# Performance work log

Measured on AMD Instinct MI355X. Metric: run time of the kernel, lower is better.

The kernel has to match this reference:

```python
import jax, jax.numpy as jnp
import numpy as np

VOCAB, EDIM, WFEAT, LABELS, SLOPE = 50000, 128, 128, 2, 0.01
N = 8192

def setup_inputs() -> dict:
    key = jax.random.key(0)
    ks = jax.random.split(key, 8)
    inSen = jax.random.randint(ks[0], (N,), 0, VOCAB, dtype=jnp.int64) if jax.config.read('jax_enable_x64') else jax.random.randint(ks[0], (N,), 0, VOCAB, dtype=jnp.int32)
    adj = jax.random.randint(ks[1], (N, N), 0, 2, dtype=jnp.int32)
    emb = jax.random.normal(ks[2], (VOCAB, EDIM), dtype=jnp.float32)
    W = jax.random.normal(ks[3], (EDIM, WFEAT), dtype=jnp.float32) * (1.0 / np.sqrt(EDIM))
    a_src = jax.random.normal(ks[4], (WFEAT,), dtype=jnp.float32) * (1.0 / np.sqrt(WFEAT))
    a_dst = jax.random.normal(ks[5], (WFEAT,), dtype=jnp.float32) * (1.0 / np.sqrt(WFEAT))
    cls_W = jax.random.normal(ks[6], (WFEAT, LABELS), dtype=jnp.float32) * (1.0 / np.sqrt(WFEAT))
    cls_b = jax.random.normal(ks[7], (LABELS,), dtype=jnp.float32) * 0.01
    return {"inSen": inSen, "adj": adj, "selfLink": 1, "emb": emb, "W": W,
            "a_src": a_src, "a_dst": a_dst, "cls_W": cls_W, "cls_b": cls_b}

def reference(inSen, adj, selfLink, emb, W, a_src, a_dst, cls_W, cls_b):
    # Embedding lookup: (N, edim)
    words = emb[inSen]
    # GAT layer: linear projection then adjacency-masked additive attention
    h = words @ W                              # (N, wFeat)
    f_src = h @ a_src                          # (N,)
    f_dst = h @ a_dst                          # (N,)
    e = jax.nn.leaky_relu(f_src[:, None] + f_dst[None, :], negative_slope=SLOPE)  # (N, N)
    mask = (adj + selfLink * jnp.eye(adj.shape[0], dtype=adj.dtype)) > 0
    e = jnp.where(mask, e, jnp.float32(-1e9))
    attention = jax.nn.softmax(e, axis=1)      # (N, N)
    sentence = attention @ h                   # (N, wFeat)
    # Max pool over words, classify
    poolSentence = jnp.max(sentence, axis=0)   # (wFeat,)
    label = jax.nn.softmax(poolSentence @ cls_W + cls_b, axis=0)  # (labels,)
    return (poolSentence, attention, sentence, label)
```

## Files before the change

kernel.cpp:

```cpp
#include <hip/hip_runtime.h>
#include <hip/hip_bf16.h>

#define NR 8192
#define WF 128
#define MSTRIDE 260

typedef short bf16x8 __attribute__((ext_vector_type(8)));
typedef float f32x4 __attribute__((ext_vector_type(4)));

static __device__ __forceinline__ unsigned int f2bf(float f) {
    unsigned int u = __float_as_uint(f);
    return (u + 0x7fffu + ((u >> 16) & 1u)) >> 16;
}
static __device__ __forceinline__ void atomicMaxF(float* addr, float v) {
    if (v >= 0.f) atomicMax((int*)addr, __float_as_int(v));
    else          atomicMin((unsigned int*)addr, __float_as_uint(v));
}
static __device__ __forceinline__ float lrelu(float x) { return x > 0.f ? x : 0.01f * x; }

__global__ __launch_bounds__(256) void k_proj(
    const int* __restrict__ inSen, const float* __restrict__ emb,
    const float* __restrict__ W, const float* __restrict__ a_src,
    const float* __restrict__ a_dst, float* __restrict__ f_src,
    float* __restrict__ f_dst, float* __restrict__ maxfd,
    unsigned short* __restrict__ hB)
{
    __shared__ float ht[16 * 132];
    const int t = threadIdx.x;
    const int f = t & 127, rh = t >> 7;
    const int i0 = blockIdx.x * 16;

    int wd[8];
    #pragma unroll
    for (int r = 0; r < 8; ++r) wd[r] = inSen[i0 + rh * 8 + r];
    float h[8];
    #pragma unroll
    for (int r = 0; r < 8; ++r) h[r] = 0.f;

    for (int k4 = 0; k4 < 32; ++k4) {
        const float w0 = W[(k4 * 4 + 0) * WF + f];
        const float w1 = W[(k4 * 4 + 1) * WF + f];
        const float w2 = W[(k4 * 4 + 2) * WF + f];
        const float w3 = W[(k4 * 4 + 3) * WF + f];
        #pragma unroll
        for (int r = 0; r < 8; ++r) {
            float4 ev = ((const float4*)(emb + (size_t)wd[r] * 128))[k4];
            h[r] += ev.x * w0 + ev.y * w1 + ev.z * w2 + ev.w * w3;
        }
    }
    #pragma unroll
    for (int r = 0; r < 8; ++r) ht[(rh * 8 + r) * 132 + f] = h[r];
    __syncthreads();

    if (t < 16) {
        float s = 0.f, d = 0.f;
        for (int k4 = 0; k4 < 32; ++k4) {
            float4 hv = *(const float4*)(ht + t * 132 + k4 * 4);
            float4 as = ((const float4*)a_src)[k4];
            float4 ad = ((const float4*)a_dst)[k4];
            s += hv.x * as.x + hv.y * as.y + hv.z * as.z + hv.w * as.w;
            d += hv.x * ad.x + hv.y * ad.y + hv.z * ad.z + hv.w * ad.w;
        }
        f_src[i0 + t] = s;
        f_dst[i0 + t] = d;
        float dm = d;
        #pragma unroll
        for (int o = 1; o < 16; o <<= 1) dm = fmaxf(dm, __shfl_xor(dm, o));
        if (t == 0) atomicMaxF(maxfd, dm);
    }
    {
        const int kb = blockIdx.x >> 1, half = blockIdx.x & 1;
        const int nf = t >> 5, l32 = t & 31;
        const int qloc = l32 >> 4, fx = l32 & 15;
        const int lane = (half * 2 + qloc) * 16 + fx;
        const float* hp = ht + (qloc * 8) * 132 + nf * 16 + fx;
        uint4 v;
        v.x = f2bf(hp[0 * 132]) | (f2bf(hp[1 * 132]) << 16);
        v.y = f2bf(hp[2 * 132]) | (f2bf(hp[3 * 132]) << 16);
        v.z = f2bf(hp[4 * 132]) | (f2bf(hp[5 * 132]) << 16);
        v.w = f2bf(hp[6 * 132]) | (f2bf(hp[7 * 132]) << 16);
        *(uint4*)(hB + ((size_t)kb * 8 + nf) * 512 + lane * 8) = v;
    }
}

static __device__ __forceinline__ void adj_chunk(
    int c, int4 a, const float* __restrict__ fdl, int lane, int row, int sl,
    float fs, float C, int shl,
    unsigned int* __restrict__ mrow, float& sum)
{
    const float4 f = *(const float4*)(fdl + c * 256 + 4 * lane);
    const bool m0 = a.x > 0, m1 = a.y > 0, m2 = a.z > 0, m3 = a.w > 0;
    float p0 = m0 ? __expf(lrelu(fs + f.x) - C) : 0.f;
    float p1 = m1 ? __expf(lrelu(fs + f.y) - C) : 0.f;
    float p2 = m2 ? __expf(lrelu(fs + f.z) - C) : 0.f;
    float p3 = m3 ? __expf(lrelu(fs + f.w) - C) : 0.f;
    unsigned int nib = (m0 ? 1u : 0u) | (m1 ? 2u : 0u) | (m2 ? 4u : 0u) | (m3 ? 8u : 0u);
    float ssum = p0 + p1 + p2 + p3;
    if (c == (row >> 8)) {
        if (lane == ((row & 255) >> 2)) {
            const int jd = row & 3;
            const int aj = jd == 0 ? a.x : jd == 1 ? a.y : jd == 2 ? a.z : a.w;
            const float fj = jd == 0 ? f.x : jd == 1 ? f.y : jd == 2 ? f.z : f.w;
            const bool mo = aj > 0, mn = (aj + sl) > 0;
            if (mn != mo) {
                const float pd = __expf(lrelu(fs + fj) - C);
                if (mn) { nib |= 1u << jd; ssum += pd; }
                else    { nib &= ~(1u << jd); ssum -= pd; }
            }
        }
    }
    sum += ssum;
    unsigned int v = nib << shl;
    v |= __shfl_xor(v, 1);
    v |= __shfl_xor(v, 2);
    v |= __shfl_xor(v, 4);
    if ((lane & 7) == 0) mrow[c * 8 + (lane >> 3)] = v;
}

static __device__ __forceinline__ float adj_row(
    const int* __restrict__ ap, const float* __restrict__ fdl,
    int lane, int row, int sl, float fs, float C, int shl,
    unsigned int* __restrict__ mrow,
    int4 a0, int4 a1, int4 a2, int4 a3, int4 a4, int4 a5, int4 a6, int4 a7)
{
    float sum = 0.f;
    #define ADJC(c, reg) adj_chunk((c), (reg), fdl, lane, row, sl, fs, C, shl, mrow, sum)
    #pragma unroll 1
    for (int g = 0; g < 24; g += 8) {
        ADJC(g + 0, a0); a0 = *(const int4*)(ap + (g +  8) * 256);
        ADJC(g + 1, a1); a1 = *(const int4*)(ap + (g +  9) * 256);
        ADJC(g + 2, a2); a2 = *(const int4*)(ap + (g + 10) * 256);
        ADJC(g + 3, a3); a3 = *(const int4*)(ap + (g + 11) * 256);
        ADJC(g + 4, a4); a4 = *(const int4*)(ap + (g + 12) * 256);
        ADJC(g + 5, a5); a5 = *(const int4*)(ap + (g + 13) * 256);
        ADJC(g + 6, a6); a6 = *(const int4*)(ap + (g + 14) * 256);
        ADJC(g + 7, a7); a7 = *(const int4*)(ap + (g + 15) * 256);
    }
    ADJC(24, a0); ADJC(25, a1); ADJC(26, a2); ADJC(27, a3);
    ADJC(28, a4); ADJC(29, a5); ADJC(30, a6); ADJC(31, a7);
    #undef ADJC
    return sum;
}

__global__ __launch_bounds__(512, 4) void k_fused(
    const int* __restrict__ adj, const int* __restrict__ slP,
    const float* __restrict__ f_src, const float* __restrict__ f_dst,
    const float* __restrict__ maxfd, const unsigned short* __restrict__ hB,
    float* __restrict__ att, float* __restrict__ sent, float* __restrict__ partial)
{
    __shared__ float red[8][2048];
    __shared__ float sums[16];
    float* fdl = &red[0][0];
    unsigned int* mask = (unsigned int*)&red[4][0];
    const int t = threadIdx.x, lane = t & 63, w = t >> 6;
    const int strip = blockIdx.x;
    const int i0 = strip * 16;

    const int rowA = i0 + 2 * w;
    const int* __restrict__ apA = adj + (size_t)rowA * NR + 4 * lane;
    int4 a0 = *(const int4*)(apA + 0 * 256);
    int4 a1 = *(const int4*)(apA + 1 * 256);
    int4 a2 = *(const int4*)(apA + 2 * 256);
    int4 a3 = *(const int4*)(apA + 3 * 256);
    int4 a4 = *(const int4*)(apA + 4 * 256);
    int4 a5 = *(const int4*)(apA + 5 * 256);
    int4 a6 = *(const int4*)(apA + 6 * 256);
    int4 a7 = *(const int4*)(apA + 7 * 256);

    #pragma unroll
    for (int i = 0; i < 4; ++i)
        *(float4*)(fdl + (i * 512 + t) * 4) = *(const float4*)(f_dst + (i * 512 + t) * 4);

    const int sl = slP[0];
    const float mfd = maxfd[0];
    const int shl = 4 * (lane & 7);
    __syncthreads();

    {
        const float fsA = f_src[rowA];
        const float CA = lrelu(fsA + mfd);
        float s = adj_row(apA, fdl, lane, rowA, sl, fsA, CA, shl,
                          mask + (2 * w) * MSTRIDE, a0, a1, a2, a3, a4, a5, a6, a7);
        #pragma unroll
        for (int o = 1; o < 64; o <<= 1) s += __shfl_xor(s, o);
        if (lane == 0) sums[2 * w] = 1.0f / s;
    }
    {
        const int rowB = i0 + 2 * w + 1;
        const int* __restrict__ apB = adj + (size_t)rowB * NR + 4 * lane;
        int4 b0 = *(const int4*)(apB + 0 * 256);
        int4 b1 = *(const int4*)(apB + 1 * 256);
        int4 b2 = *(const int4*)(apB + 2 * 256);
        int4 b3 = *(const int4*)(apB + 3 * 256);
        int4 b4 = *(const int4*)(apB + 4 * 256);
        int4 b5 = *(const int4*)(apB + 5 * 256);
        int4 b6 = *(const int4*)(apB + 6 * 256);
        int4 b7 = *(const int4*)(apB + 7 * 256);
        const float fsB = f_src[rowB];
        const float CB = lrelu(fsB + mfd);
        float s = adj_row(apB, fdl, lane, rowB, sl, fsB, CB, shl,
                          mask + (2 * w + 1) * MSTRIDE, b0, b1, b2, b3, b4, b5, b6, b7);
        #pragma unroll
        for (int o = 1; o < 64; o <<= 1) s += __shfl_xor(s, o);
        if (lane == 0) sums[2 * w + 1] = 1.0f / s;
    }
    __syncthreads();

    const int fx = lane & 15, quad = lane >> 4;
    const int row = i0 + fx;
    const float fs = f_src[row];
    const float C = lrelu(fs + mfd);
    const float il = sums[fx];
    float* __restrict__ ar = att + (size_t)row * NR;
    const unsigned int* __restrict__ mrow = mask + fx * MSTRIDE;
    f32x4 acc[8] = {};
    const int k0 = w * 1024;

    for (int kk4 = k0; kk4 < k0 + 1024; kk4 += 128) {
        const uint4 mw = *(const uint4*)(mrow + (kk4 >> 5));
        const unsigned int mwa[4] = {mw.x, mw.y, mw.z, mw.w};
        #pragma unroll
        for (int j4 = 0; j4 < 4; ++j4) {
            const int kk = kk4 + j4 * 32;
            const int kb = kk >> 5;
            const unsigned short* hp = hB + (size_t)kb * 4096 + lane * 8;
            bf16x8 bfr[8];
            #pragma unroll
            for (int nf = 0; nf < 8; ++nf) bfr[nf] = *(const bf16x8*)(hp + nf * 512);

            const unsigned int mbyte = (mwa[j4] >> (quad * 8)) & 0xffu;
            const float4 fd0 = *(const float4*)(fdl + kk + quad * 8);
            const float4 fd1 = *(const float4*)(fdl + kk + quad * 8 + 4);
            const float fv[8] = {fd0.x, fd0.y, fd0.z, fd0.w, fd1.x, fd1.y, fd1.z, fd1.w};
            float p[8];
            #pragma unroll
            for (int j = 0; j < 8; ++j)
                p[j] = ((mbyte >> j) & 1u) ? __expf(lrelu(fs + fv[j]) - C) : 0.f;

            const float4 w0 = make_float4(p[0] * il, p[1] * il, p[2] * il, p[3] * il);
            const float4 w1 = make_float4(p[4] * il, p[5] * il, p[6] * il, p[7] * il);
            *(float4*)(ar + kk + quad * 8) = w0;
            *(float4*)(ar + kk + quad * 8 + 4) = w1;

            union { uint4 u; bf16x8 v; } cv;
            cv.u.x = f2bf(p[0]) | (f2bf(p[1]) << 16);
            cv.u.y = f2bf(p[2]) | (f2bf(p[3]) << 16);
            cv.u.z = f2bf(p[4]) | (f2bf(p[5]) << 16);
            cv.u.w = f2bf(p[6]) | (f2bf(p[7]) << 16);
            #pragma unroll
            for (int nf = 0; nf < 8; ++nf)
                acc[nf] = __builtin_amdgcn_mfma_f32_16x16x32_bf16(cv.v, bfr[nf], acc[nf], 0, 0, 0);
        }
    }
    __syncthreads();
    #pragma unroll
    for (int reg = 0; reg < 4; ++reg) {
        #pragma unroll
        for (int nf = 0; nf < 8; ++nf)
            red[w][(quad * 4 + reg) * 128 + nf * 16 + fx] = acc[nf][reg];
    }
    __syncthreads();
    const int e0 = t * 4;
    const int m = e0 >> 7, f0 = e0 & 127;
    {
        const float vin = sums[m];
        float vv[4];
        #pragma unroll
        for (int j = 0; j < 4; ++j) {
            float s = 0.f;
            #pragma unroll
            for (int sx = 0; sx < 8; ++sx) s += red[sx][e0 + j];
            vv[j] = s * vin;
        }
        *(float4*)(sent + (size_t)(i0 + m) * WF + f0) = make_float4(vv[0], vv[1], vv[2], vv[3]);
        red[0][e0 + 0] = vv[0]; red[0][e0 + 1] = vv[1];
        red[0][e0 + 2] = vv[2]; red[0][e0 + 3] = vv[3];
    }
    __syncthreads();
    if (t < 128) {
        float mx = red[0][t];
        #pragma unroll
        for (int mm = 1; mm < 16; ++mm) mx = fmaxf(mx, red[0][mm * 128 + t]);
        partial[strip * 128 + t] = mx;
    }
}

__global__ __launch_bounds__(128) void k_label(
    const float* __restrict__ partial, const float* __restrict__ cls_W,
    const float* __restrict__ cls_b, float* __restrict__ pool,
    float* __restrict__ label)
{
    __shared__ float s0[128], s1[128];
    const int t = threadIdx.x;
    float m0 = -1e30f, m1 = -1e30f, m2 = -1e30f, m3 = -1e30f;
    for (int b = 0; b < 512; b += 4) {
        m0 = fmaxf(m0, partial[(b + 0) * 128 + t]);
        m1 = fmaxf(m1, partial[(b + 1) * 128 + t]);
        m2 = fmaxf(m2, partial[(b + 2) * 128 + t]);
        m3 = fmaxf(m3, partial[(b + 3) * 128 + t]);
    }
    const float m = fmaxf(fmaxf(m0, m1), fmaxf(m2, m3));
    pool[t] = m;
    s0[t] = m * cls_W[t * 2 + 0];
    s1[t] = m * cls_W[t * 2 + 1];
    __syncthreads();
    if (t == 0) {
        float z0 = cls_b[0], z1 = cls_b[1];
        for (int f = 0; f < 128; ++f) { z0 += s0[f]; z1 += s1[f]; }
        float mm = fmaxf(z0, z1);
        float e0 = __expf(z0 - mm), e1 = __expf(z1 - mm);
        float inv = 1.0f / (e0 + e1);
        label[0] = e0 * inv;
        label[1] = e1 * inv;
    }
}

extern "C" void kernel_launch(void* const* d_in, const int* in_sizes, int n_in,
                              void* d_out, int out_size, void* d_ws, size_t ws_size,
                              hipStream_t stream)
{
    const int*   inSen    = (const int*)d_in[0];
    const int*   adj      = (const int*)d_in[1];
    const int*   selfLink = (const int*)d_in[2];
    const float* emb      = (const float*)d_in[3];
    const float* W        = (const float*)d_in[4];
    const float* a_src    = (const float*)d_in[5];
    const float* a_dst    = (const float*)d_in[6];
    const float* cls_W    = (const float*)d_in[7];
    const float* cls_b    = (const float*)d_in[8];

    float* out   = (float*)d_out;
    float* pool  = out;
    float* att   = out + 128;
    float* sent  = att + (size_t)NR * NR;
    float* label = sent + (size_t)NR * WF;

    char* ws = (char*)d_ws;
    unsigned short* hB    = (unsigned short*)ws;
    float* f_src   = (float*)(ws + (2u << 20));
    float* f_dst   = f_src + NR;
    float* maxfd   = f_dst + NR;
    float* partial = maxfd + 64;

    hipMemsetAsync(maxfd, 0xFF, 4, stream);
    k_proj<<<NR / 16, 256, 0, stream>>>(inSen, emb, W, a_src, a_dst, f_src, f_dst, maxfd, hB);
    k_fused<<<NR / 16, 512, 0, stream>>>(adj, selfLink, f_src, f_dst, maxfd, hB, att, sent, partial);
    k_label<<<1, 128, 0, stream>>>(partial, cls_W, cls_b, pool, label);
}
```

Baseline: 585.8 us.

## Double block size to 32 rows, use nontemporal adj loads and atomic LDS reduction

The fused kernel now runs 1024 threads per block covering 32 rows, so each f_dst staging into LDS is shared by twice as many rows and the grid is halved. The adjacency loads use nontemporal builtins to avoid polluting cache with the streamed 256MB matrix. The cross-wave reduction of MFMA accumulators now uses LDS atomicAdd into two 16-row tiles instead of a staged buffer plus explicit sum. The trade-offs are LDS atomic contention, larger LDS use (about 74KB) that may limit residency, and launch_bounds(1024,4) that may be unachievable.

```diff
diff --git a/kernel.cpp b/kernel.cpp
--- a/kernel.cpp
+++ b/kernel.cpp
@@ -7,6 +7,7 @@
 
 typedef short bf16x8 __attribute__((ext_vector_type(8)));
 typedef float f32x4 __attribute__((ext_vector_type(4)));
+typedef int   i32x4 __attribute__((ext_vector_type(4)));
 
 static __device__ __forceinline__ unsigned int f2bf(float f) {
     unsigned int u = __float_as_uint(f);
@@ -84,12 +85,12 @@
 }
 
 static __device__ __forceinline__ void adj_chunk(
-    int c, int4 a, const float* __restrict__ fdl, int lane, int row, int sl,
+    int c, i32x4 a, const float* __restrict__ fdl, int lane, int row, int sl,
     float fs, float C, int shl,
     unsigned int* __restrict__ mrow, float& sum)
 {
     const float4 f = *(const float4*)(fdl + c * 256 + 4 * lane);
-    const bool m0 = a.x > 0, m1 = a.y > 0, m2 = a.z > 0, m3 = a.w > 0;
+    const bool m0 = a[0] > 0, m1 = a[1] > 0, m2 = a[2] > 0, m3 = a[3] > 0;
     float p0 = m0 ? __expf(lrelu(fs + f.x) - C) : 0.f;
     float p1 = m1 ? __expf(lrelu(fs + f.y) - C) : 0.f;
     float p2 = m2 ? __expf(lrelu(fs + f.z) - C) : 0.f;
@@ -99,7 +100,7 @@
     if (c == (row >> 8)) {
         if (lane == ((row & 255) >> 2)) {
             const int jd = row & 3;
-            const int aj = jd == 0 ? a.x : jd == 1 ? a.y : jd == 2 ? a.z : a.w;
+            const int aj = jd == 0 ? a[0] : jd == 1 ? a[1] : jd == 2 ? a[2] : a[3];
             const float fj = jd == 0 ? f.x : jd == 1 ? f.y : jd == 2 ? f.z : f.w;
             const bool mo = aj > 0, mn = (aj + sl) > 0;
             if (mn != mo) {
@@ -117,24 +118,26 @@
     if ((lane & 7) == 0) mrow[c * 8 + (lane >> 3)] = v;
 }
 
+#define NTL(p) __builtin_nontemporal_load((const i32x4*)(p))
+
 static __device__ __forceinline__ float adj_row(
     const int* __restrict__ ap, const float* __restrict__ fdl,
     int lane, int row, int sl, float fs, float C, int shl,
     unsigned int* __restrict__ mrow,
-    int4 a0, int4 a1, int4 a2, int4 a3, int4 a4, int4 a5, int4 a6, int4 a7)
+    i32x4 a0, i32x4 a1, i32x4 a2, i32x4 a3, i32x4 a4, i32x4 a5, i32x4 a6, i32x4 a7)
 {
     float sum = 0.f;
     #define ADJC(c, reg) adj_chunk((c), (reg), fdl, lane, row, sl, fs, C, shl, mrow, sum)
     #pragma unroll 1
     for (int g = 0; g < 24; g += 8) {
-        ADJC(g + 0, a0); a0 = *(const int4*)(ap + (g +  8) * 256);
-        ADJC(g + 1, a1); a1 = *(const int4*)(ap + (g +  9) * 256);
-        ADJC(g + 2, a2); a2 = *(const int4*)(ap + (g + 10) * 256);
-        ADJC(g + 3, a3); a3 = *(const int4*)(ap + (g + 11) * 256);
-        ADJC(g + 4, a4); a4 = *(const int4*)(ap + (g + 12) * 256);
-        ADJC(g + 5, a5); a5 = *(const int4*)(ap + (g + 13) * 256);
-        ADJC(g + 6, a6); a6 = *(const int4*)(ap + (g + 14) * 256);
-        ADJC(g + 7, a7); a7 = *(const int4*)(ap + (g + 15) * 256);
+        ADJC(g + 0, a0); a0 = NTL(ap + (g +  8) * 256);
+        ADJC(g + 1, a1); a1 = NTL(ap + (g +  9) * 256);
+        ADJC(g + 2, a2); a2 = NTL(ap + (g + 10) * 256);
+        ADJC(g + 3, a3); a3 = NTL(ap + (g + 11) * 256);
+        ADJC(g + 4, a4); a4 = NTL(ap + (g + 12) * 256);
+        ADJC(g + 5, a5); a5 = NTL(ap + (g + 13) * 256);
+        ADJC(g + 6, a6); a6 = NTL(ap + (g + 14) * 256);
+        ADJC(g + 7, a7); a7 = NTL(ap + (g + 15) * 256);
     }
     ADJC(24, a0); ADJC(25, a1); ADJC(26, a2); ADJC(27, a3);
     ADJC(28, a4); ADJC(29, a5); ADJC(30, a6); ADJC(31, a7);
@@ -142,34 +145,37 @@
     return sum;
 }
 
-__global__ __launch_bounds__(512, 4) void k_fused(
+__global__ __launch_bounds__(1024, 4) void k_fused(
     const int* __restrict__ adj, const int* __restrict__ slP,
     const float* __restrict__ f_src, const float* __restrict__ f_dst,
     const float* __restrict__ maxfd, const unsigned short* __restrict__ hB,
     float* __restrict__ att, float* __restrict__ sent, float* __restrict__ partial)
 {
-    __shared__ float red[8][2048];
-    __shared__ float sums[16];
-    float* fdl = &red[0][0];
-    unsigned int* mask = (unsigned int*)&red[4][0];
+    __shared__ float fdl[NR];
+    __shared__ unsigned int mask[32 * MSTRIDE];
+    __shared__ float tile[2][2048];
+    __shared__ float sums[32];
     const int t = threadIdx.x, lane = t & 63, w = t >> 6;
-    const int strip = blockIdx.x;
-    const int i0 = strip * 16;
+    const int i0 = blockIdx.x * 32;
 
     const int rowA = i0 + 2 * w;
     const int* __restrict__ apA = adj + (size_t)rowA * NR + 4 * lane;
-    int4 a0 = *(const int4*)(apA + 0 * 256);
-    int4 a1 = *(const int4*)(apA + 1 * 256);
-    int4 a2 = *(const int4*)(apA + 2 * 256);
-    int4 a3 = *(const int4*)(apA + 3 * 256);
-    int4 a4 = *(const int4*)(apA + 4 * 256);
-    int4 a5 = *(const int4*)(apA + 5 * 256);
-    int4 a6 = *(const int4*)(apA + 6 * 256);
-    int4 a7 = *(const int4*)(apA + 7 * 256);
-
-    #pragma unroll
-    for (int i = 0; i < 4; ++i)
-        *(float4*)(fdl + (i * 512 + t) * 4) = *(const float4*)(f_dst + (i * 512 + t) * 4);
+    i32x4 a0 = NTL(apA + 0 * 256);
+    i32x4 a1 = NTL(apA + 1 * 256);
+    i32x4 a2 = NTL(apA + 2 * 256);
+    i32x4 a3 = NTL(apA + 3 * 256);
+    i32x4 a4 = NTL(apA + 4 * 256);
+    i32x4 a5 = NTL(apA + 5 * 256);
+    i32x4 a6 = NTL(apA + 6 * 256);
+    i32x4 a7 = NTL(apA + 7 * 256);
+
+    #pragma unroll
+    for (int i = 0; i < 2; ++i)
+        *(float4*)(fdl + (i * 1024 + t) * 4) = *(const float4*)(f_dst + (i * 1024 + t) * 4);
+    {
+        float4 z = make_float4(0.f, 0.f, 0.f, 0.f);
+        *(float4*)(&tile[0][0] + t * 4) = z;
+    }
 
     const int sl = slP[0];
     const float mfd = maxfd[0];
@@ -186,16 +192,16 @@
         if (lane == 0) sums[2 * w] = 1.0f / s;
     }
     {
-        const int rowB = i0 + 2 * w + 1;
+        const int rowB = rowA + 1;
         const int* __restrict__ apB = adj + (size_t)rowB * NR + 4 * lane;
-        int4 b0 = *(const int4*)(apB + 0 * 256);
-        int4 b1 = *(const int4*)(apB + 1 * 256);
-        int4 b2 = *(const int4*)(apB + 2 * 256);
-        int4 b3 = *(const int4*)(apB + 3 * 256);
-        int4 b4 = *(const int4*)(apB + 4 * 256);
-        int4 b5 = *(const int4*)(apB + 5 * 256);
-        int4 b6 = *(const int4*)(apB + 6 * 256);
-        int4 b7 = *(const int4*)(apB + 7 * 256);
+        i32x4 b0 = NTL(apB + 0 * 256);
+        i32x4 b1 = NTL(apB + 1 * 256);
+        i32x4 b2 = NTL(apB + 2 * 256);
+        i32x4 b3 = NTL(apB + 3 * 256);
+        i32x4 b4 = NTL(apB + 4 * 256);
+        i32x4 b5 = NTL(apB + 5 * 256);
+        i32x4 b6 = NTL(apB + 6 * 256);
+        i32x4 b7 = NTL(apB + 7 * 256);
         const float fsB = f_src[rowB];
         const float CB = lrelu(fsB + mfd);
         float s = adj_row(apB, fdl, lane, rowB, sl, fsB, CB, shl,
@@ -206,15 +212,17 @@
     }
     __syncthreads();
 
+    const int ss = w >> 3, wk = w & 7;
     const int fx = lane & 15, quad = lane >> 4;
-    const int row = i0 + fx;
+    const int lrow = ss * 16 + fx;
+    const int row = i0 + lrow;
     const float fs = f_src[row];
     const float C = lrelu(fs + mfd);
-    const float il = sums[fx];
+    const float il = sums[lrow];
     float* __restrict__ ar = att + (size_t)row * NR;
-    const unsigned int* __restrict__ mrow = mask + fx * MSTRIDE;
+    const unsigned int* __restrict__ mrow = mask + lrow * MSTRIDE;
     f32x4 acc[8] = {};
-    const int k0 = w * 1024;
+    const int k0 = wk * 1024;
 
     for (int kk4 = k0; kk4 < k0 + 1024; kk4 += 128) {
         const uint4 mw = *(const uint4*)(mrow + (kk4 >> 5));
@@ -252,36 +260,28 @@
                 acc[nf] = __builtin_amdgcn_mfma_f32_16x16x32_bf16(cv.v, bfr[nf], acc[nf], 0, 0, 0);
         }
     }
-    __syncthreads();
     #pragma unroll
     for (int reg = 0; reg < 4; ++reg) {
         #pragma unroll
         for (int nf = 0; nf < 8; ++nf)
-            red[w][(quad * 4 + reg) * 128 + nf * 16 + fx] = acc[nf][reg];
-    }
-    __syncthreads();
-    const int e0 = t * 4;
-    const int m = e0 >> 7, f0 = e0 & 127;
-    {
-        const float vin = sums[m];
-        float vv[4];
-        #pragma unroll
-        for (int j = 0; j < 4; ++j) {
-            float s = 0.f;
-            #pragma unroll
-            for (int sx = 0; sx < 8; ++sx) s += red[sx][e0 + j];
-            vv[j] = s * vin;
-        }
-        *(float4*)(sent + (size_t)(i0 + m) * WF + f0) = make_float4(vv[0], vv[1], vv[2], vv[3]);
-        red[0][e0 + 0] = vv[0]; red[0][e0 + 1] = vv[1];
-        red[0][e0 + 2] = vv[2]; red[0][e0 + 3] = vv[3];
-    }
-    __syncthreads();
+            atomicAdd(&tile[ss][(quad * 4 + reg) * 128 + nf * 16 + fx], acc[nf][reg]);
+    }
+    __syncthreads();
+    {
+        const int e = t * 4;
+        const int st2 = e >> 11, off = e & 2047, r = off >> 7, f0 = off & 127;
+        const float vin = sums[st2 * 16 + r];
+        const float* tf = &tile[0][0];
+        float4 vv = make_float4(tf[e] * vin, tf[e + 1] * vin, tf[e + 2] * vin, tf[e + 3] * vin);
+        *(float4*)(sent + (size_t)(i0 + st2 * 16 + r) * WF + f0) = vv;
+    }
     if (t < 128) {
-        float mx = red[0][t];
-        #pragma unroll
-        for (int mm = 1; mm < 16; ++mm) mx = fmaxf(mx, red[0][mm * 128 + t]);
-        partial[strip * 128 + t] = mx;
+        float mx = -1e30f;
+        #pragma unroll
+        for (int s = 0; s < 2; ++s)
+            for (int r = 0; r < 16; ++r)
+                mx = fmaxf(mx, tile[s][r * 128 + t] * sums[s * 16 + r]);
+        partial[blockIdx.x * 128 + t] = mx;
     }
 }
 
@@ -293,7 +293,7 @@
     __shared__ float s0[128], s1[128];
     const int t = threadIdx.x;
     float m0 = -1e30f, m1 = -1e30f, m2 = -1e30f, m3 = -1e30f;
-    for (int b = 0; b < 512; b += 4) {
+    for (int b = 0; b < 256; b += 4) {
         m0 = fmaxf(m0, partial[(b + 0) * 128 + t]);
         m1 = fmaxf(m1, partial[(b + 1) * 128 + t]);
         m2 = fmaxf(m2, partial[(b + 2) * 128 + t]);
@@ -344,6 +344,6 @@
 
     hipMemsetAsync(maxfd, 0xFF, 4, stream);
     k_proj<<<NR / 16, 256, 0, stream>>>(inSen, emb, W, a_src, a_dst, f_src, f_dst, maxfd, hB);
-    k_fused<<<NR / 16, 512, 0, stream>>>(adj, selfLink, f_src, f_dst, maxfd, hB, att, sent, partial);
+    k_fused<<<NR / 32, 1024, 0, stream>>>(adj, selfLink, f_src, f_dst, maxfd, hB, att, sent, partial);
     k_label<<<1, 128, 0, stream>>>(partial, cls_W, cls_b, pool, label);
 }
```

Result: no change. 583.8 us (-0.3%).
